# Optimization experiments

Measured on AMD Instinct MI355X. Metric: run time of the kernel, lower is better.

## Reference

```python
import math
import jax, jax.numpy as jnp
import numpy as np

NUM_BUCKETS = 32
MAX_DISTANCE = 128
N_HEADS = 16
D_KV = 64


def relative_position_bucket(rel_pos, num_buckets=NUM_BUCKETS, max_distance=MAX_DISTANCE):
    # bidirectional=True path of the original
    n = -rel_pos
    nb = num_buckets // 2
    ret = (n < 0).astype(jnp.int32) * nb
    n = jnp.abs(n)
    max_exact = nb // 2
    is_small = n < max_exact
    val_large = max_exact + (
        jnp.log(n.astype(jnp.float32) / max_exact)
        / math.log(max_distance / max_exact)
        * (nb - max_exact)
    ).astype(jnp.int32)
    val_large = jnp.minimum(val_large, nb - 1)
    return jnp.where(is_small, n, val_large) + ret


def setup_inputs() -> dict:
    key = jax.random.key(0)
    ks = jax.random.split(key, 6)
    B, S, D = 2, 2048, 1024
    inner = N_HEADS * D_KV  # 1024
    sc = 1.0 / math.sqrt(D)
    return {
        "x": jax.random.normal(ks[0], (B, S, D), dtype=jnp.float32),
        "Wq": jax.random.normal(ks[1], (D, inner), dtype=jnp.float32) * sc,
        "Wk": jax.random.normal(ks[2], (D, inner), dtype=jnp.float32) * sc,
        "Wv": jax.random.normal(ks[3], (D, inner), dtype=jnp.float32) * sc,
        "Wo": jax.random.normal(ks[4], (inner, D), dtype=jnp.float32) * sc,
        "rel_table": jax.random.normal(ks[5], (NUM_BUCKETS, N_HEADS), dtype=jnp.float32),
        "attention_mask": jnp.zeros((B, 1, 1, S), dtype=jnp.float32),
    }


def reference(x, Wq, Wk, Wv, Wo, rel_table, attention_mask):
    B, S, D = x.shape
    H, Dk = N_HEADS, D_KV

    q = (x @ Wq).reshape(B, S, H, Dk).transpose(0, 2, 1, 3)  # bhqd
    k = (x @ Wk).reshape(B, S, H, Dk).transpose(0, 2, 1, 3)
    v = (x @ Wv).reshape(B, S, H, Dk).transpose(0, 2, 1, 3)

    # NOTE: T5 attention has no 1/sqrt(d) scaling
    scores = jnp.einsum('bhqd,bhkd->bhqk', q.astype(jnp.float32), k.astype(jnp.float32))

    pos = jnp.arange(S)
    rel_pos = pos[None, :] - pos[:, None]  # [S,S] = k_pos - q_pos
    buckets = relative_position_bucket(rel_pos)
    position_bias = jnp.transpose(rel_table[buckets], (2, 0, 1))  # [H,S,S]

    scores = scores + position_bias[None, ...] + attention_mask
    weights = jax.nn.softmax(scores, axis=-1)
    out = jnp.einsum('bhqk,bhkd->bhqd', weights, v.astype(jnp.float32))
    out = out.transpose(0, 2, 1, 3).reshape(B, S, H * Dk).astype(x.dtype)
    out = out @ Wo
    return (out, position_bias)
```

## Files before the change

kernel.cpp:

```cpp
#include <hip/hip_runtime.h>
#include <hip/hip_bf16.h>
#include <math.h>
#include <stdint.h>

typedef __bf16 bf16_t;
typedef __attribute__((ext_vector_type(8))) __bf16 bf16x8;
typedef __attribute__((ext_vector_type(4))) float f32x4;
typedef unsigned short u16;
typedef unsigned int u32;

#define DEV static __device__ __forceinline__
#define LOG2E 1.4426950408889634f

DEV u16 f2b(float f){ bf16_t h = (bf16_t)f; return __builtin_bit_cast(u16, h); }
DEV float b2f(u16 u){ bf16_t h = __builtin_bit_cast(bf16_t, u); return (float)h; }
DEV f32x4 mfma16(bf16x8 a, bf16x8 b, f32x4 c){
  return __builtin_amdgcn_mfma_f32_16x16x32_bf16(a, b, c, 0, 0, 0);
}

#if __has_builtin(__builtin_amdgcn_exp2f)
DEV float fexp2(float x){ return __builtin_amdgcn_exp2f(x); }
#else
DEV float fexp2(float x){ return exp2f(x); }
#endif

DEV void gld16(const void* g, void* l){
  __builtin_amdgcn_global_load_lds((const __attribute__((address_space(1))) u32*)g,
                                   (__attribute__((address_space(3))) u32*)l, 16, 0, 0);
}

DEV bf16x8 ldsA64(const u16* arr, int row, int ch){
  return *(const bf16x8*)&arr[row*64 + ((ch ^ (row&7))*8)];
}
DEV bf16x8 ldsA32(const u16* arr, int row, int ch){
  return *(const bf16x8*)&arr[row*32 + ((ch ^ ((row>>1)&3))*8)];
}

__global__ __launch_bounds__(256) void k_convert_x(const float* __restrict__ x,
                                                   u16* __restrict__ xh, u16* __restrict__ xl){
  size_t i = ((size_t)blockIdx.x*256 + threadIdx.x)*4;
  float4 v = *(const float4*)(x + i);
  ushort4 hv, lv; float f, hf;
  f=v.x; hv.x=f2b(f); hf=b2f(hv.x); lv.x=f2b(f-hf);
  f=v.y; hv.y=f2b(f); hf=b2f(hv.y); lv.y=f2b(f-hf);
  f=v.z; hv.z=f2b(f); hf=b2f(hv.z); lv.z=f2b(f-hf);
  f=v.w; hv.w=f2b(f); hf=b2f(hv.w); lv.w=f2b(f-hf);
  *(ushort4*)(xh+i) = hv;
  *(ushort4*)(xl+i) = lv;
}

__global__ __launch_bounds__(256) void k_convert_w(const float* __restrict__ Wq, const float* __restrict__ Wk,
                                                   const float* __restrict__ Wv, const float* __restrict__ Wo,
                                                   u16* __restrict__ wth, u16* __restrict__ wtl,
                                                   u16* __restrict__ wot){
  __shared__ float tile[64][65];
  int z = blockIdx.z;
  const float* W = (z==0)?Wq:((z==1)?Wk:((z==2)?Wv:Wo));
  int n0 = blockIdx.x*64, k0 = blockIdx.y*64;
  int t = threadIdx.x;
  int r = t>>6, c = t&63;
  #pragma unroll
  for(int i=0;i<16;i++){
    int row = i*4 + r;
    tile[row][c] = W[(size_t)(k0+row)*1024 + n0 + c];
  }
  __syncthreads();
  #pragma unroll
  for(int i=0;i<16;i++){
    int nrow = i*4 + r;
    float v = tile[c][nrow];
    size_t o = (size_t)(n0+nrow)*1024 + k0 + c;
    u16 hb = f2b(v);
    if(z<3){
      wth[(size_t)z*1048576 + o] = hb;
      wtl[(size_t)z*1048576 + o] = f2b(v - b2f(hb));
    } else {
      wot[o] = hb;
    }
  }
}

__global__ __launch_bounds__(256) void k_bias_table(const float* __restrict__ rel_table,
                                                    const float* __restrict__ mask,
                                                    float* __restrict__ bt, float* __restrict__ bt2,
                                                    float* __restrict__ msk2){
  int gid = blockIdx.x*256 + threadIdx.x;
  if(gid < 4096) msk2[gid] = mask[gid]*LOG2E;
  int h = gid >> 12, idx = gid & 4095;
  float v = 0.f;
  if(idx < 4095){
    int delta = idx - 2047;
    int n = -delta;
    int ret = 0;
    if(n < 0){ ret = 16; n = -n; }
    int bucket;
    if(n < 8) bucket = n + ret;
    else {
      float a = (float)log((double)n * 0.125);
      float rr = (float)((double)a / (double)2.7725887298583984f);
      int vl = 8 + (int)(rr * 8.0f);
      vl = vl > 15 ? 15 : vl;
      bucket = vl + ret;
    }
    v = rel_table[bucket*16 + h];
  }
  bt[gid] = v;
  bt2[gid] = v*LOG2E - 32.0f;
}

__global__ __launch_bounds__(256) void k_write_bias(const float* __restrict__ bt,
                                                    float* __restrict__ out){
  size_t f = ((size_t)blockIdx.x*256 + threadIdx.x)*4;
  int h = (int)(f >> 22);
  int rem = (int)(f & 4194303);
  int q = rem >> 11;
  int k = rem & 2047;
  const float* row = bt + h*4096 + (k - q + 2047);
  float4 v = make_float4(row[0], row[1], row[2], row[3]);
  *(float4*)(out + f) = v;
}

__global__ __launch_bounds__(256) void k_gemm_qkv(const u16* __restrict__ xh, const u16* __restrict__ xl,
                                                  const u16* __restrict__ wth, const u16* __restrict__ wtl,
                                                  u16* __restrict__ qh, u16* __restrict__ ql,
                                                  u16* __restrict__ kh, u16* __restrict__ vt){
  __shared__ __align__(16) u16 SM[17408];
  u16* Ah = SM; u16* Al = SM+4096; u16* Bh = SM+8192; u16* Bl = SM+12288;
  int z = blockIdx.z;
  const u16* WH = wth + (size_t)z*1048576;
  const u16* WL = wtl + (size_t)z*1048576;
  int m0 = blockIdx.y*128, n0 = blockIdx.x*128;
  int t = threadIdx.x, w = t>>6, lane = t&63, l16 = lane&15, g = lane>>4;
  const f32x4 fzero = {0.f,0.f,0.f,0.f};
  f32x4 acc[4][4];
  #pragma unroll
  for(int i=0;i<4;i++)
    #pragma unroll
    for(int j=0;j<4;j++) acc[i][j] = fzero;
  int rbase = (w>>1)*64, cbase = (w&1)*64;
  for(int k0=0;k0<1024;k0+=32){
    __syncthreads();
    #pragma unroll
    for(int jj=0;jj<8;jj++){
      int q = w + 4*jj;
      int arr = q>>3, sub = q&7;
      if(z==2 && (arr&1)) continue;
      int row = sub*16 + (lane>>2);
      int lch = (lane&3) ^ ((row>>1)&3);
      const u16* src;
      if(arr==0)      src = xh + (size_t)(m0+row)*1024 + k0 + lch*8;
      else if(arr==1) src = xl + (size_t)(m0+row)*1024 + k0 + lch*8;
      else if(arr==2) src = WH + (size_t)(n0+row)*1024 + k0 + lch*8;
      else            src = WL + (size_t)(n0+row)*1024 + k0 + lch*8;
      gld16(src, &SM[q*512]);
    }
    __syncthreads();
    if(z==2){
      bf16x8 ah[4];
      #pragma unroll
      for(int i=0;i<4;i++) ah[i] = ldsA32(Ah, rbase + i*16 + l16, g);
      #pragma unroll
      for(int j=0;j<4;j++){
        bf16x8 bh = ldsA32(Bh, cbase + j*16 + l16, g);
        #pragma unroll
        for(int i=0;i<4;i++)
          acc[i][j] = mfma16(ah[i], bh, acc[i][j]);
      }
    } else {
      bf16x8 ah[4], am[4];
      #pragma unroll
      for(int i=0;i<4;i++){
        int row = rbase + i*16 + l16;
        ah[i] = ldsA32(Ah, row, g);
        am[i] = ldsA32(Al, row, g);
      }
      #pragma unroll
      for(int j=0;j<4;j++){
        int row = cbase + j*16 + l16;
        bf16x8 bh = ldsA32(Bh, row, g);
        bf16x8 bl = ldsA32(Bl, row, g);
        #pragma unroll
        for(int i=0;i<4;i++){
          acc[i][j] = mfma16(ah[i], bh, acc[i][j]);
          acc[i][j] = mfma16(ah[i], bl, acc[i][j]);
          acc[i][j] = mfma16(am[i], bh, acc[i][j]);
        }
      }
    }
  }
  if(z==2){
    __syncthreads();
    #pragma unroll
    for(int i=0;i<4;i++)
      #pragma unroll
      for(int j=0;j<4;j++)
        #pragma unroll
        for(int r=0;r<4;r++){
          int ml = rbase + i*16 + g*4 + r;
          int nl = cbase + j*16 + l16;
          SM[nl*136 + ml] = f2b(acc[i][j][r]);
        }
    __syncthreads();
    int bb = m0 >> 11;
    #pragma unroll
    for(int kk=0;kk<8;kk++){
      int id = t + 256*kk;
      int row = id>>4, ch = id&15;
      uint4 v = *(const uint4*)&SM[row*136 + ch*8];
      int n = n0 + row;
      size_t dst = ((size_t)(bb*16 + (n>>6))*64 + (n&63))*2048 + (m0&2047) + ch*8;
      *(uint4*)&vt[dst] = v;
    }
  } else {
    #pragma unroll
    for(int i=0;i<4;i++)
      #pragma unroll
      for(int j=0;j<4;j++)
        #pragma unroll
        for(int r=0;r<4;r++){
          int m = m0 + rbase + i*16 + g*4 + r;
          int n = n0 + cbase + j*16 + l16;
          float v = acc[i][j][r];
          if(z==0) v *= LOG2E;
          int b = m >> 11, s = m & 2047;
          int hh = n >> 6, d = n & 63;
          size_t a = ((size_t)(b*16+hh)*2048 + s)*64 + d;
          u16 hb = f2b(v);
          if(z==0){ qh[a]=hb; ql[a]=f2b(v - b2f(hb)); }
          else    { kh[a]=hb; }
        }
  }
}

__global__ __launch_bounds__(256) void k_attn(const u16* __restrict__ qh, const u16* __restrict__ ql,
                                              const u16* __restrict__ kh,
                                              const u16* __restrict__ vt, const float* __restrict__ bt2,
                                              const float* __restrict__ msk2, u16* __restrict__ ao){
  __shared__ __align__(16) u16 SM[17408];
  u16* KH = SM; u16* VT = SM+4096;
  int bh = blockIdx.y, b = bh>>4, h = bh&15;
  int q0 = blockIdx.x*128;
  int t = threadIdx.x, w = t>>6, lane = t&63, l16 = lane&15, g = lane>>4;
  size_t base  = (size_t)bh*2048*64;
  size_t vbase = (size_t)bh*64*2048;
  u16* PSw = SM + 8192 + w*2304;
  const float* bt2h = bt2 + h*4096;
  const float* msk2b = msk2 + b*2048;

  bf16x8 qfh[2][2], qfl[2][2];
  #pragma unroll
  for(int i=0;i<2;i++){
    int qr = q0 + w*32 + i*16 + l16;
    size_t a0 = base + (size_t)qr*64 + g*8;
    qfh[i][0] = *(const bf16x8*)&qh[a0];
    qfl[i][0] = *(const bf16x8*)&ql[a0];
    qfh[i][1] = *(const bf16x8*)&qh[a0+32];
    qfl[i][1] = *(const bf16x8*)&ql[a0+32];
  }
  f32x4 O[2][4];
  float rs[2][4];
  #pragma unroll
  for(int i=0;i<2;i++){
    #pragma unroll
    for(int jd=0;jd<4;jd++) O[i][jd] = {0.f,0.f,0.f,0.f};
    #pragma unroll
    for(int r=0;r<4;r++) rs[i][r] = 0.f;
  }

  for(int k0=0;k0<2048;k0+=64){
    __syncthreads();
    #pragma unroll
    for(int jj=0;jj<4;jj++){
      int q = w + 4*jj;
      int arr = q>>3, sub = q&7;
      int row = sub*8 + (lane>>3);
      int lch = (lane&7) ^ (row&7);
      const u16* src;
      if(arr==0) src = kh + base + (size_t)(k0+row)*64 + lch*8;
      else       src = vt + vbase + (size_t)row*2048 + k0 + lch*8;
      gld16(src, &SM[q*512]);
    }
    float mkj[4];
    #pragma unroll
    for(int j=0;j<4;j++) mkj[j] = msk2b[k0 + j*16 + l16];
    f32x4 sc[2][4];
    #pragma unroll
    for(int i=0;i<2;i++){
      const float* bb = bt2h + (k0 + l16 + 2047 - (q0 + w*32 + i*16 + g*4));
      #pragma unroll
      for(int j=0;j<4;j++){
        #pragma unroll
        for(int r=0;r<4;r++)
          sc[i][j][r] = bb[j*16 - r] + mkj[j];
      }
    }
    __syncthreads();
    #pragma unroll
    for(int j=0;j<4;j++){
      int krow = j*16 + l16;
      bf16x8 kfh0 = ldsA64(KH, krow, g);
      bf16x8 kfh1 = ldsA64(KH, krow, 4+g);
      #pragma unroll
      for(int i=0;i<2;i++){
        f32x4 s = sc[i][j];
        s = mfma16(qfh[i][0], kfh0, s);
        s = mfma16(qfl[i][0], kfh0, s);
        s = mfma16(qfh[i][1], kfh1, s);
        s = mfma16(qfl[i][1], kfh1, s);
        sc[i][j] = s;
      }
    }
    #pragma unroll
    for(int i=0;i<2;i++){
      #pragma unroll
      for(int j=0;j<4;j++){
        #pragma unroll
        for(int r=0;r<4;r++){
          float p = fexp2(sc[i][j][r]);
          rs[i][r] += p;
          PSw[(i*16 + g*4 + r)*72 + j*16 + l16] = f2b(p);
        }
      }
    }
    #pragma unroll
    for(int ds=0; ds<2; ds++){
      bf16x8 pa0 = *(const bf16x8*)&PSw[(     l16)*72 + ds*32 + g*8];
      bf16x8 pa1 = *(const bf16x8*)&PSw[(16 + l16)*72 + ds*32 + g*8];
      #pragma unroll
      for(int jd=0;jd<4;jd++){
        bf16x8 vb = ldsA64(VT, jd*16 + l16, ds*4 + g);
        O[0][jd] = mfma16(pa0, vb, O[0][jd]);
        O[1][jd] = mfma16(pa1, vb, O[1][jd]);
      }
    }
  }
  #pragma unroll
  for(int i=0;i<2;i++){
    float inv[4];
    #pragma unroll
    for(int r=0;r<4;r++){
      float v = rs[i][r];
      v += __shfl_xor(v,1,64);
      v += __shfl_xor(v,2,64);
      v += __shfl_xor(v,4,64);
      v += __shfl_xor(v,8,64);
      inv[r] = 1.f/v;
    }
    #pragma unroll
    for(int r=0;r<4;r++){
      int q = q0 + w*32 + i*16 + g*4 + r;
      size_t a = ((size_t)(b*2048 + q))*1024 + h*64;
      #pragma unroll
      for(int jd=0;jd<4;jd++)
        ao[a + jd*16 + l16] = f2b(O[i][jd][r]*inv[r]);
    }
  }
}

__global__ __launch_bounds__(256) void k_gemm_out(const u16* __restrict__ ao, const u16* __restrict__ wot,
                                                  float* __restrict__ out){
  __shared__ __align__(16) u16 SM[8192];
  u16* As = SM; u16* Bs = SM+4096;
  int m0 = blockIdx.y*128, n0 = blockIdx.x*128;
  int t = threadIdx.x, w = t>>6, lane = t&63, l16 = lane&15, g = lane>>4;
  f32x4 acc[4][4];
  #pragma unroll
  for(int i=0;i<4;i++)
    #pragma unroll
    for(int j=0;j<4;j++) acc[i][j] = {0.f,0.f,0.f,0.f};
  int rbase = (w>>1)*64, cbase = (w&1)*64;
  for(int k0=0;k0<1024;k0+=32){
    __syncthreads();
    #pragma unroll
    for(int jj=0;jj<4;jj++){
      int q = w + 4*jj;
      int arr = q>>3, sub = q&7;
      int row = sub*16 + (lane>>2);
      int lch = (lane&3) ^ ((row>>1)&3);
      const u16* src;
      if(arr==0) src = ao  + (size_t)(m0+row)*1024 + k0 + lch*8;
      else       src = wot + (size_t)(n0+row)*1024 + k0 + lch*8;
      gld16(src, &SM[q*512]);
    }
    __syncthreads();
    bf16x8 af[4];
    #pragma unroll
    for(int i=0;i<4;i++) af[i] = ldsA32(As, rbase + i*16 + l16, g);
    #pragma unroll
    for(int j=0;j<4;j++){
      bf16x8 bfb = ldsA32(Bs, cbase + j*16 + l16, g);
      #pragma unroll
      for(int i=0;i<4;i++)
        acc[i][j] = mfma16(af[i], bfb, acc[i][j]);
    }
  }
  #pragma unroll
  for(int i=0;i<4;i++)
    #pragma unroll
    for(int j=0;j<4;j++)
      #pragma unroll
      for(int r=0;r<4;r++){
        int m = m0 + rbase + i*16 + g*4 + r;
        int n = n0 + cbase + j*16 + l16;
        out[(size_t)m*1024 + n] = acc[i][j][r];
      }
}

extern "C" void kernel_launch(void* const* d_in, const int* in_sizes, int n_in,
                              void* d_out, int out_size, void* d_ws, size_t ws_size,
                              hipStream_t stream) {
  const float* x   = (const float*)d_in[0];
  const float* Wq  = (const float*)d_in[1];
  const float* Wk  = (const float*)d_in[2];
  const float* Wv  = (const float*)d_in[3];
  const float* Wo  = (const float*)d_in[4];
  const float* rel = (const float*)d_in[5];
  const float* msk = (const float*)d_in[6];
  float* out = (float*)d_out;
  float* bias_out = out + (size_t)4194304;
  char* ws = (char*)d_ws;
  u16* xh  = (u16*)(ws + 0);
  u16* xl  = (u16*)(ws + 8388608);
  u16* wth = (u16*)(ws + 16777216);
  u16* wtl = (u16*)(ws + 23068672);
  u16* wot = (u16*)(ws + 29360128);
  u16* qh  = (u16*)(ws + 31457280);
  u16* ql  = (u16*)(ws + 39845888);
  u16* kh  = (u16*)(ws + 48234496);
  u16* vt  = (u16*)(ws + 65011712);
  u16* ao  = (u16*)(ws + 73400320);
  float* bt   = (float*)(ws + 81788928);
  float* bt2  = (float*)(ws + 82051072);
  float* msk2 = (float*)(ws + 82313216);

  k_convert_x <<<4096, 256, 0, stream>>>(x, xh, xl);
  k_convert_w <<<dim3(16,16,4), 256, 0, stream>>>(Wq, Wk, Wv, Wo, wth, wtl, wot);
  k_bias_table<<<256, 256, 0, stream>>>(rel, msk, bt, bt2, msk2);
  k_write_bias<<<65536, 256, 0, stream>>>(bt, bias_out);
  k_gemm_qkv  <<<dim3(8,32,3), 256, 0, stream>>>(xh, xl, wth, wtl, qh, ql, kh, vt);
  k_attn      <<<dim3(16,32), 256, 0, stream>>>(qh, ql, kh, vt, bt2, msk2, ao);
  k_gemm_out  <<<dim3(8,32), 256, 0, stream>>>(ao, wot, out);
}
```

Measured before the change: 532.2 us.

## Split attention over key halves and drop weight low-part in QKV GEMM

Attention is split across two key-range halves via a third grid dimension, writing unnormalized fp32 partial outputs and row sums that a new combine kernel sums, normalizes and packs to bf16. Since the row max appears fixed (constant offset baked into the bias), partials can be added directly. Separately, the QKV projection drops the low-order bf16 part of the weights, cutting one MFMA per tile step and a quarter of the loads. The split doubles attention occupancy (512 to 1024 blocks) at the cost of extra fp32 partial traffic; dropping weight precision may loosen accuracy.

```diff
diff --git a/kernel.cpp b/kernel.cpp
--- a/kernel.cpp
+++ b/kernel.cpp
@@ -51,8 +51,7 @@
 
 __global__ __launch_bounds__(256) void k_convert_w(const float* __restrict__ Wq, const float* __restrict__ Wk,
                                                    const float* __restrict__ Wv, const float* __restrict__ Wo,
-                                                   u16* __restrict__ wth, u16* __restrict__ wtl,
-                                                   u16* __restrict__ wot){
+                                                   u16* __restrict__ wth, u16* __restrict__ wot){
   __shared__ float tile[64][65];
   int z = blockIdx.z;
   const float* W = (z==0)?Wq:((z==1)?Wk:((z==2)?Wv:Wo));
@@ -70,13 +69,8 @@
     int nrow = i*4 + r;
     float v = tile[c][nrow];
     size_t o = (size_t)(n0+nrow)*1024 + k0 + c;
-    u16 hb = f2b(v);
-    if(z<3){
-      wth[(size_t)z*1048576 + o] = hb;
-      wtl[(size_t)z*1048576 + o] = f2b(v - b2f(hb));
-    } else {
-      wot[o] = hb;
-    }
+    if(z<3) wth[(size_t)z*1048576 + o] = f2b(v);
+    else    wot[o] = f2b(v);
   }
 }
 
@@ -121,37 +115,34 @@
 }
 
 __global__ __launch_bounds__(256) void k_gemm_qkv(const u16* __restrict__ xh, const u16* __restrict__ xl,
-                                                  const u16* __restrict__ wth, const u16* __restrict__ wtl,
+                                                  const u16* __restrict__ wth,
                                                   u16* __restrict__ qh, u16* __restrict__ ql,
                                                   u16* __restrict__ kh, u16* __restrict__ vt){
   __shared__ __align__(16) u16 SM[17408];
-  u16* Ah = SM; u16* Al = SM+4096; u16* Bh = SM+8192; u16* Bl = SM+12288;
+  u16* Ah = SM; u16* Al = SM+4096; u16* Bh = SM+8192;
   int z = blockIdx.z;
   const u16* WH = wth + (size_t)z*1048576;
-  const u16* WL = wtl + (size_t)z*1048576;
   int m0 = blockIdx.y*128, n0 = blockIdx.x*128;
   int t = threadIdx.x, w = t>>6, lane = t&63, l16 = lane&15, g = lane>>4;
-  const f32x4 fzero = {0.f,0.f,0.f,0.f};
   f32x4 acc[4][4];
   #pragma unroll
   for(int i=0;i<4;i++)
     #pragma unroll
-    for(int j=0;j<4;j++) acc[i][j] = fzero;
+    for(int j=0;j<4;j++) acc[i][j] = {0.f,0.f,0.f,0.f};
   int rbase = (w>>1)*64, cbase = (w&1)*64;
   for(int k0=0;k0<1024;k0+=32){
     __syncthreads();
     #pragma unroll
-    for(int jj=0;jj<8;jj++){
+    for(int jj=0;jj<6;jj++){
       int q = w + 4*jj;
       int arr = q>>3, sub = q&7;
-      if(z==2 && (arr&1)) continue;
+      if(z==2 && arr==1) continue;
       int row = sub*16 + (lane>>2);
       int lch = (lane&3) ^ ((row>>1)&3);
       const u16* src;
       if(arr==0)      src = xh + (size_t)(m0+row)*1024 + k0 + lch*8;
       else if(arr==1) src = xl + (size_t)(m0+row)*1024 + k0 + lch*8;
-      else if(arr==2) src = WH + (size_t)(n0+row)*1024 + k0 + lch*8;
-      else            src = WL + (size_t)(n0+row)*1024 + k0 + lch*8;
+      else            src = WH + (size_t)(n0+row)*1024 + k0 + lch*8;
       gld16(src, &SM[q*512]);
     }
     __syncthreads();
@@ -176,13 +167,10 @@
       }
       #pragma unroll
       for(int j=0;j<4;j++){
-        int row = cbase + j*16 + l16;
-        bf16x8 bh = ldsA32(Bh, row, g);
-        bf16x8 bl = ldsA32(Bl, row, g);
+        bf16x8 bh = ldsA32(Bh, cbase + j*16 + l16, g);
         #pragma unroll
         for(int i=0;i<4;i++){
           acc[i][j] = mfma16(ah[i], bh, acc[i][j]);
-          acc[i][j] = mfma16(ah[i], bl, acc[i][j]);
           acc[i][j] = mfma16(am[i], bh, acc[i][j]);
         }
       }
@@ -235,11 +223,13 @@
 __global__ __launch_bounds__(256) void k_attn(const u16* __restrict__ qh, const u16* __restrict__ ql,
                                               const u16* __restrict__ kh,
                                               const u16* __restrict__ vt, const float* __restrict__ bt2,
-                                              const float* __restrict__ msk2, u16* __restrict__ ao){
+                                              const float* __restrict__ msk2,
+                                              float* __restrict__ Op, float* __restrict__ rsp){
   __shared__ __align__(16) u16 SM[17408];
   u16* KH = SM; u16* VT = SM+4096;
   int bh = blockIdx.y, b = bh>>4, h = bh&15;
   int q0 = blockIdx.x*128;
+  int kha = blockIdx.z;
   int t = threadIdx.x, w = t>>6, lane = t&63, l16 = lane&15, g = lane>>4;
   size_t base  = (size_t)bh*2048*64;
   size_t vbase = (size_t)bh*64*2048;
@@ -267,7 +257,8 @@
     for(int r=0;r<4;r++) rs[i][r] = 0.f;
   }
 
-  for(int k0=0;k0<2048;k0+=64){
+  int kend = kha*1024 + 1024;
+  for(int k0=kha*1024; k0<kend; k0+=64){
     __syncthreads();
     #pragma unroll
     for(int jj=0;jj<4;jj++){
@@ -334,9 +325,9 @@
       }
     }
   }
+  size_t pbase = ((size_t)kha*32 + bh)*2048;
   #pragma unroll
   for(int i=0;i<2;i++){
-    float inv[4];
     #pragma unroll
     for(int r=0;r<4;r++){
       float v = rs[i][r];
@@ -344,17 +335,32 @@
       v += __shfl_xor(v,2,64);
       v += __shfl_xor(v,4,64);
       v += __shfl_xor(v,8,64);
-      inv[r] = 1.f/v;
-    }
-    #pragma unroll
-    for(int r=0;r<4;r++){
       int q = q0 + w*32 + i*16 + g*4 + r;
-      size_t a = ((size_t)(b*2048 + q))*1024 + h*64;
+      size_t oo = (pbase + q)*64;
       #pragma unroll
       for(int jd=0;jd<4;jd++)
-        ao[a + jd*16 + l16] = f2b(O[i][jd][r]*inv[r]);
-    }
-  }
+        Op[oo + jd*16 + l16] = O[i][jd][r];
+      if(l16==0) rsp[pbase + q] = v;
+    }
+  }
+}
+
+__global__ __launch_bounds__(256) void k_combine(const float* __restrict__ Op, const float* __restrict__ rsp,
+                                                 u16* __restrict__ ao){
+  size_t fid = ((size_t)blockIdx.x*256 + threadIdx.x)*4;
+  int m = (int)(fid >> 10), n = (int)(fid & 1023);
+  int bh = (m>>11)*16 + (n>>6);
+  int q = m & 2047, d = n & 63;
+  size_t po = ((size_t)bh*2048 + q)*64 + d;
+  f32x4 a = *(const f32x4*)&Op[po];
+  f32x4 c = *(const f32x4*)&Op[po + 4194304];
+  float inv = 1.f/(rsp[bh*2048 + q] + rsp[bh*2048 + q + 65536]);
+  ushort4 o;
+  o.x = f2b((a[0]+c[0])*inv);
+  o.y = f2b((a[1]+c[1])*inv);
+  o.z = f2b((a[2]+c[2])*inv);
+  o.w = f2b((a[3]+c[3])*inv);
+  *(ushort4*)&ao[fid] = o;
 }
 
 __global__ __launch_bounds__(256) void k_gemm_out(const u16* __restrict__ ao, const u16* __restrict__ wot,
@@ -422,22 +428,24 @@
   u16* xh  = (u16*)(ws + 0);
   u16* xl  = (u16*)(ws + 8388608);
   u16* wth = (u16*)(ws + 16777216);
-  u16* wtl = (u16*)(ws + 23068672);
-  u16* wot = (u16*)(ws + 29360128);
-  u16* qh  = (u16*)(ws + 31457280);
-  u16* ql  = (u16*)(ws + 39845888);
-  u16* kh  = (u16*)(ws + 48234496);
-  u16* vt  = (u16*)(ws + 65011712);
-  u16* ao  = (u16*)(ws + 73400320);
-  float* bt   = (float*)(ws + 81788928);
-  float* bt2  = (float*)(ws + 82051072);
-  float* msk2 = (float*)(ws + 82313216);
+  u16* wot = (u16*)(ws + 23068672);
+  u16* qh  = (u16*)(ws + 25165824);
+  u16* ql  = (u16*)(ws + 33554432);
+  u16* kh  = (u16*)(ws + 41943040);
+  u16* vt  = (u16*)(ws + 50331648);
+  u16* ao  = (u16*)(ws + 58720256);
+  float* Op  = (float*)(ws + 67108864);
+  float* rsp = (float*)(ws + 100663296);
+  float* bt  = (float*)(ws + 101187584);
+  float* bt2 = (float*)(ws + 101449728);
+  float* msk2= (float*)(ws + 101711872);
 
   k_convert_x <<<4096, 256, 0, stream>>>(x, xh, xl);
-  k_convert_w <<<dim3(16,16,4), 256, 0, stream>>>(Wq, Wk, Wv, Wo, wth, wtl, wot);
+  k_convert_w <<<dim3(16,16,4), 256, 0, stream>>>(Wq, Wk, Wv, Wo, wth, wot);
   k_bias_table<<<256, 256, 0, stream>>>(rel, msk, bt, bt2, msk2);
   k_write_bias<<<65536, 256, 0, stream>>>(bt, bias_out);
-  k_gemm_qkv  <<<dim3(8,32,3), 256, 0, stream>>>(xh, xl, wth, wtl, qh, ql, kh, vt);
-  k_attn      <<<dim3(16,32), 256, 0, stream>>>(qh, ql, kh, vt, bt2, msk2, ao);
+  k_gemm_qkv  <<<dim3(8,32,3), 256, 0, stream>>>(xh, xl, wth, qh, ql, kh, vt);
+  k_attn      <<<dim3(16,32,2), 256, 0, stream>>>(qh, ql, kh, vt, bt2, msk2, Op, rsp);
+  k_combine   <<<4096, 256, 0, stream>>>(Op, rsp, ao);
   k_gemm_out  <<<dim3(8,32), 256, 0, stream>>>(ao, wot, out);
 }
```

Result: faster. 517.2 us (-2.8%).
